# Performance work log

Hardware: AMD Instinct MI355X
Metric: run time of the kernel (lower is better)

The kernel has to match this reference:

```python
import jax, jax.numpy as jnp
import numpy as np

B, S, D = 8, 1024, 2048      # batch, seq_len, output_dim
M = 2048                     # memory_len
N = 9                        # internal n_turns = user n_turns (8) + 1
C = 2                        # compression_rate
N_CONV = sum(C ** i for i in range(1, N))  # 510; long-memory helix capacity


def _avg_pool(x, c):
    # Non-overlapping avg pool over time, window=stride=c.
    # Equivalent to the original tile->avg_pool1d->[..., :D] (tiling repeats
    # channels, and the first D channels of the pooled tile equal pooling x).
    b, l, d = x.shape
    return x.reshape(b, l // c, c, d).mean(axis=2)


def setup_inputs() -> dict:
    key = jax.random.key(0)
    k1, k2 = jax.random.split(key)
    inputs = jax.random.normal(k1, (B, S, D), dtype=jnp.float32)
    memory = jax.random.normal(k2, (B, M + N_CONV, D), dtype=jnp.float32)
    return {"inputs": inputs, "memory": memory}


def reference(inputs, memory):
    short_start = C ** N  # 512
    new_memory = jnp.concatenate([memory, inputs], axis=1)  # [B, M+N_CONV+S, D]
    short_memory = new_memory[:, short_start:short_start + M]  # [B, M, D]
    long_memory = new_memory[:, :short_start]                  # [B, C^N, D]
    fallout = short_memory[:, :S]
    sh_fallout = _avg_pool(fallout, C)                         # [B, S//C, D]
    helix = jnp.concatenate([long_memory, sh_fallout], axis=1)

    parts = []
    for k in range(1, N):  # small fixed unroll over helix turns
        turn_end = C ** (N - k)
        turn_start = helix.shape[1] - turn_end
        old = helix[:, turn_start:]            # [B, C^(N-k), D]
        comp = _avg_pool(old, C)               # [B, C^(N-k-1), D]
        helix = jnp.concatenate([helix[:, :turn_start], comp], axis=1)
        # new k-th turn: drop oldest comp-length entries, append compression
        parts.append(jnp.concatenate([old[:, comp.shape[1]:], comp], axis=1))

    # new_mem = [part_{N-1}, ..., part_1, short_memory]
    new_mem = jnp.concatenate(parts[::-1] + [short_memory], axis=1)
    return new_mem  # [B, M + N_CONV, D]
```

## Files before the change

kernel.cpp:

```cpp
#include <hip/hip_runtime.h>


typedef __attribute__((ext_vector_type(4))) float f32x4;

#define B_    8
#define D_    2048
#define MEMR_ 2558
#define OUTR_ 2558
#define INR_  1024

#define POOL_DT     64
#define POOL_BLOCKS (B_ * POOL_DT)
#define COPY_BLOCKS (B_ * 2048)

__device__ __forceinline__ void write_row(float* dst, const float* s, float scale) {
  f32x4 o;
#pragma unroll
  for (int e = 0; e < 4; ++e) o[e] = s[e] * scale;
  __builtin_nontemporal_store(o, reinterpret_cast<f32x4*>(dst));
}

__global__ __launch_bounds__(256) void helix_kernel(
    const float* __restrict__ inputs,
    const float* __restrict__ memory,
    float* __restrict__ out) {
  __shared__ float lds[32 * 32];
  const int bid = blockIdx.x;
  const int tid = threadIdx.x;

  if (bid < POOL_BLOCKS) {
    const int b  = bid >> 6;
    const int dt = bid & 63;
    const int q  = tid >> 3;
    const int c  = tid & 7;
    const int dcol = dt * 32 + c * 4;

    const float* fall = memory + ((long)b * MEMR_ + 1024) * D_ + dcol;
    float* ob = out + (long)b * OUTR_ * D_ + dcol;

    float f[4], s1[4], s2[4], s3[4], s4[4];
    const float* rp = fall + (long)(q * 16) * D_;

#pragma unroll
    for (int j = 0; j < 16; ++j) {
      f32x4 u = *reinterpret_cast<const f32x4*>(rp + (long)j * D_);
#pragma unroll
      for (int e = 0; e < 4; ++e) f[e] = u[e];
      if ((j & 1) == 0) {
#pragma unroll
        for (int e = 0; e < 4; ++e) s1[e] = f[e];
      } else {
#pragma unroll
        for (int e = 0; e < 4; ++e) s1[e] += f[e];
        const int i1 = 256 + 8 * q + (j >> 1);
        if (i1 >= 384) write_row(ob + (long)(i1 - 130) * D_, s1, 0.5f);
        if ((j & 3) == 1) {
#pragma unroll
          for (int e = 0; e < 4; ++e) s2[e] = s1[e];
        } else {
#pragma unroll
          for (int e = 0; e < 4; ++e) s2[e] += s1[e];
          const int i2 = 128 + 4 * q + (j >> 2);
          write_row(ob + (long)(254 + i2) * D_, s2, 0.25f);
          if (i2 >= 192) write_row(ob + (long)(i2 - 66) * D_, s2, 0.25f);
          if ((j & 7) == 3) {
#pragma unroll
            for (int e = 0; e < 4; ++e) s3[e] = s2[e];
          } else {
#pragma unroll
            for (int e = 0; e < 4; ++e) s3[e] += s2[e];
            const int i3 = 64 + 2 * q + (j >> 3);
            write_row(ob + (long)(126 + i3) * D_, s3, 0.125f);
            if (i3 >= 96) write_row(ob + (long)(i3 - 34) * D_, s3, 0.125f);
            if (j == 7) {
#pragma unroll
              for (int e = 0; e < 4; ++e) s4[e] = s3[e];
            } else if (j == 15) {
#pragma unroll
              for (int e = 0; e < 4; ++e) s4[e] += s3[e];
              const int i4 = 32 + q;
              write_row(ob + (long)(62 + i4) * D_, s4, 0.0625f);
              if (i4 >= 48) write_row(ob + (long)(i4 - 18) * D_, s4, 0.0625f);
            }
          }
        }
      }
    }

    float* myl = lds + q * 32 + c * 4;
#pragma unroll
    for (int e = 0; e < 4; ++e) myl[e] = s4[e];

    int nq = 16;
    float scale = 1.0f / 32.0f;
    for (int l = 5; l <= 9; ++l) {
      __syncthreads();
      float a[4], bb[4];
      const bool act = (q < nq);
      if (act) {
#pragma unroll
        for (int e = 0; e < 4; ++e) {
          a[e]  = lds[(2 * q) * 32 + c * 4 + e];
          bb[e] = lds[(2 * q + 1) * 32 + c * 4 + e];
        }
      }
      __syncthreads();
      if (act) {
#pragma unroll
        for (int e = 0; e < 4; ++e) a[e] += bb[e];
#pragma unroll
        for (int e = 0; e < 4; ++e) lds[q * 32 + c * 4 + e] = a[e];
        const int i = nq + q;
        write_row(ob + (long)((1 << (10 - l)) - 2 + i) * D_, a, scale);
        if (l < 9 && i >= (3 << (8 - l)))
          write_row(ob + (long)((1 << (9 - l)) - 2 + i - (3 << (8 - l))) * D_, a, scale);
      }
      nq >>= 1;
      scale *= 0.5f;
    }
  } else {
    const int bid2 = bid - POOL_BLOCKS;
    const int b = bid2 >> 11;
    const int j = bid2 & 2047;
    const float* src = (j < 2046)
        ? memory + ((long)b * MEMR_ + 512 + j) * D_
        : inputs + ((long)b * INR_ + (j - 2046)) * D_;
    float* dst = out + ((long)b * OUTR_ + 510 + j) * D_;
    const f32x4* s4p = reinterpret_cast<const f32x4*>(src);
    f32x4* d4p = reinterpret_cast<f32x4*>(dst);
    f32x4 v0 = __builtin_nontemporal_load(s4p + tid);
    f32x4 v1 = __builtin_nontemporal_load(s4p + tid + 256);
    __builtin_nontemporal_store(v0, d4p + tid);
    __builtin_nontemporal_store(v1, d4p + tid + 256);
  }
}

extern "C" void kernel_launch(void* const* d_in, const int* in_sizes, int n_in,
                              void* d_out, int out_size, void* d_ws, size_t ws_size,
                              hipStream_t stream) {
  const float* inputs = (const float*)d_in[0];
  const float* memory = (const float*)d_in[1];
  float* out = (float*)d_out;
  helix_kernel<<<dim3(POOL_BLOCKS + COPY_BLOCKS), dim3(256), 0, stream>>>(inputs, memory, out);
}
```

Measured before the change: 296.5 us.

## Reuse fallout loads for short-memory copy and batch copy blocks with ILP

The pooling blocks already read the 512 fallout rows, so they now also write those rows straight into the short-memory output. The copy blocks therefore skip them and cover only the remaining 1536 rows per batch. Copy work moves from one block per row to 2048 blocks that each handle 3072 float4 chunks, issuing four loads before the stores, to add memory-level parallelism and cut block overhead. The index math uses a multiply-shift divide by 3 and unsigned 32-bit offsets, which adds integer work and depends on those offsets staying in range.

```diff
diff --git a/kernel.cpp b/kernel.cpp
--- a/kernel.cpp
+++ b/kernel.cpp
@@ -11,7 +11,8 @@
 
 #define POOL_DT     64
 #define POOL_BLOCKS (B_ * POOL_DT)
-#define COPY_BLOCKS (B_ * 2048)
+#define COPY_BLOCKS 2048
+#define CHUNKS_PER_BLOCK 3072
 
 __device__ __forceinline__ void write_row(float* dst, const float* s, float scale) {
   f32x4 o;
@@ -36,7 +37,8 @@
     const int dcol = dt * 32 + c * 4;
 
     const float* fall = memory + ((long)b * MEMR_ + 1024) * D_ + dcol;
-    float* ob = out + (long)b * OUTR_ * D_ + dcol;
+    float* ob  = out + (long)b * OUTR_ * D_ + dcol;
+    float* ob2 = out + ((long)b * OUTR_ + 1022) * D_ + dcol;
 
     float f[4], s1[4], s2[4], s3[4], s4[4];
     const float* rp = fall + (long)(q * 16) * D_;
@@ -44,6 +46,7 @@
 #pragma unroll
     for (int j = 0; j < 16; ++j) {
       f32x4 u = *reinterpret_cast<const f32x4*>(rp + (long)j * D_);
+      __builtin_nontemporal_store(u, reinterpret_cast<f32x4*>(ob2 + (long)(q * 16 + j) * D_));
 #pragma unroll
       for (int e = 0; e < 4; ++e) f[e] = u[e];
       if ((j & 1) == 0) {
@@ -120,18 +123,35 @@
     }
   } else {
     const int bid2 = bid - POOL_BLOCKS;
-    const int b = bid2 >> 11;
-    const int j = bid2 & 2047;
-    const float* src = (j < 2046)
-        ? memory + ((long)b * MEMR_ + 512 + j) * D_
-        : inputs + ((long)b * INR_ + (j - 2046)) * D_;
-    float* dst = out + ((long)b * OUTR_ + 510 + j) * D_;
-    const f32x4* s4p = reinterpret_cast<const f32x4*>(src);
-    f32x4* d4p = reinterpret_cast<f32x4*>(dst);
-    f32x4 v0 = __builtin_nontemporal_load(s4p + tid);
-    f32x4 v1 = __builtin_nontemporal_load(s4p + tid + 256);
-    __builtin_nontemporal_store(v0, d4p + tid);
-    __builtin_nontemporal_store(v1, d4p + tid + 256);
+    const unsigned base = (unsigned)bid2 * (unsigned)CHUNKS_PER_BLOCK;
+    const f32x4* mem4 = reinterpret_cast<const f32x4*>(memory);
+    const f32x4* in4  = reinterpret_cast<const f32x4*>(inputs);
+    f32x4* out4 = reinterpret_cast<f32x4*>(out);
+
+#pragma unroll 1
+    for (int it = 0; it < 3; ++it) {
+      f32x4 val[4];
+      unsigned dd[4];
+#pragma unroll
+      for (int k = 0; k < 4; ++k) {
+        const unsigned g  = base + (unsigned)(it * 4 + k) * 256u + (unsigned)tid;
+        const unsigned vr = g >> 9;
+        const unsigned c  = g & 511u;
+        const unsigned t  = vr >> 9;
+        const unsigned b  = (t * 21846u) >> 16;
+        const unsigned rs = vr - b * 1536u;
+        const unsigned j  = rs + ((rs >= 512u) ? 512u : 0u);
+        const unsigned d  = (b * (unsigned)MEMR_ + 510u + j) * 512u + c;
+        dd[k] = d;
+        const f32x4* sp = (j < 2046u)
+            ? (mem4 + (d + 1024u))
+            : (in4 + (((b << 10) + (j - 2046u)) * 512u + c));
+        val[k] = __builtin_nontemporal_load(sp);
+      }
+#pragma unroll
+      for (int k = 0; k < 4; ++k)
+        __builtin_nontemporal_store(val[k], out4 + dd[k]);
+    }
   }
 }
 
```

Result: no change. 299.3 us (+0.9%).
